# Kernel optimization log

Hardware: AMD Instinct MI355X
Metric: run time of the kernel (lower is better)

The kernel has to match this reference:

```python
import jax, jax.numpy as jnp
import numpy as np
import math

B, P, N, DM, H, DK, DH, DF = 2, 12, 170, 64, 8, 8, 32, 256
SQ = math.sqrt(DK)

def _ln(x, g, b):
    m = jnp.mean(x, -1, keepdims=True)
    v = jnp.var(x, -1, keepdims=True)
    return (x - m) / jnp.sqrt(v + 1e-5) * g + b

def _nozero_softmax(s):
    # faithful to nozero_softmax: mask = (s != 0), max over full row, +1e-5 in denom
    mask = (s != 0).astype(s.dtype)
    e = jnp.exp(s - jnp.max(s, -1, keepdims=True)) * mask
    return e / (jnp.sum(e, -1, keepdims=True) + 1e-5)

def _meta(c, w1, b1, w2, b2):
    # MetaLearner: [B,P,N,DM] -> [3,B,P,N,H,DK,DM]
    h = jax.nn.relu(c @ w1 + b1) @ w2 + b2
    h = h.reshape(c.shape[:3] + (3, H, DK, DM))
    return jnp.moveaxis(h, 3, 0)

def _mhlin(W, x):
    # multihead_linear_transform: per-position meta weight applied to x
    return jnp.einsum('bpnhkd,bpnd->bpnhk', W, x)

def _gdc(data, W1, W2):
    # Gated_Dynamic_Connection (noGC=False). data: [G,B,P,N,C]
    d = jnp.moveaxis(data, 0, 3)  # [B,P,N,G,C]
    a = jnp.einsum('bpngc,gcd->bpngd', d, W1)
    s = jax.nn.softmax(jax.nn.relu(jnp.einsum('bpngc,gcd->bpngd', d, W2)), axis=3)
    return jnp.sum(a * s, axis=3)  # [B,P,N,DM]

def _swish_gate(x, out, wg, bg, wo, bo):
    h = (x @ wg + bg) * out
    return (h * jax.nn.sigmoid(h)) @ wo + bo

def _spatial(Q, K, V, T):
    # adjacency-masked spatial attention. Dense-masked form is exactly the
    # scatter-into-zeros buffer of the original: zero where T==0, QK/sqrt(dk) on edges.
    s = jnp.einsum('bpihk,bpjhk->bphij', Q, K) / SQ
    Tb = T if T.ndim == 2 else T[:, :, None]  # adaptive graph [B,P,1,N,N]
    s = s * (Tb != 0)
    alpha = _nozero_softmax(s) * Tb
    return jnp.einsum('bphij,bpjhk->hbpik', alpha, V)  # [H,B,P,N,DK]

def _temporal(Q, K, V):
    s = jnp.einsum('bqnhk,bpnhk->bnhqp', Q, K) / SQ
    alpha = jax.nn.softmax(s, -1)
    return jnp.einsum('bnhqp,bpnhk->hbqnk', alpha, V)  # [H,B,P,N,DK]

def _retnet(Q, K, V, D):
    # multihead_temporal_regnet with g=1 leading dim folded in
    r = jnp.einsum('bqnhk,bpnhk->bnhqp', Q, K) / SQ
    r = r * D  # D: [H,P,P] causal decay
    rs = jnp.maximum(jnp.abs(jnp.sum(r, -1, keepdims=True)), 1.0)
    r = r / rs
    return jnp.einsum('bnhqp,bpnhk->hbqnk', r, V)  # [H,B,P,N,DK]

def _forward(x, c_x, enc, T, A, D, mr_w1, mr_b1, mr_w2, mr_b2, ms0_w1, ms0_b1, ms0_w2, ms0_b2, ms1_w1, ms1_b1, ms1_w2, ms1_b2, gr_W1, gr_W2, gs0_W1, gs0_W2, gs1_W1, gs1_W2, g2_W1, g2_W2, ge_W1, ge_W2, swr_wg, swr_bg, swr_wo, swr_bo, sws_wg, sws_bg, sws_wo, sws_bo, swe_wg, swe_bg, swe_wo, swe_bo, lnr_g, lnr_b, lns_g, lns_b, lne_g, lne_b, lnf_g, lnf_b, wq, wk, wv, f_w1, f_b1, f_w2, f_b2):
    # 1) RetNet-style temporal self retention (meta-learned QKV)
    W = _meta(c_x, mr_w1, mr_b1, mr_w2, mr_b2)
    o = _gdc(_retnet(_mhlin(W[0], x), _mhlin(W[1], x), _mhlin(W[2], x), D), gr_W1, gr_W2)
    o = _swish_gate(x, o, swr_wg, swr_bg, swr_wo, swr_bo)
    x1 = _ln(o + x, lnr_g, lnr_b)
    # 2) Spatial self attention: predefined graph + adaptive graph branches
    W0 = _meta(c_x, ms0_w1, ms0_b1, ms0_w2, ms0_b2)
    o0 = _gdc(_spatial(_mhlin(W0[0], x1), _mhlin(W0[1], x1), _mhlin(W0[2], x1), T), gs0_W1, gs0_W2)
    W1m = _meta(c_x, ms1_w1, ms1_b1, ms1_w2, ms1_b2)
    o1 = _gdc(_spatial(_mhlin(W1m[0], x1), _mhlin(W1m[1], x1), _mhlin(W1m[2], x1), A), gs1_W1, gs1_W2)
    o = _gdc(jnp.stack([o0, o1], 0), g2_W1, g2_W2)
    o = _swish_gate(x1, o, sws_wg, sws_bg, sws_wo, sws_bo)
    x2 = _ln(o + x1, lns_g, lns_b)
    # 3) Temporal encoder-decoder attention
    q = (x2 @ wq).reshape(B, P, N, H, DK)
    k = (enc @ wk).reshape(B, P, N, H, DK)
    v = (enc @ wv).reshape(B, P, N, H, DK)
    o = _gdc(_temporal(q, k, v), ge_W1, ge_W2)
    o = _swish_gate(x2, o, swe_wg, swe_bg, swe_wo, swe_bo)
    x3 = _ln(o + x2, lne_g, lne_b)
    # 4) FFN
    o = jax.nn.relu(x3 @ f_w1 + f_b1) @ f_w2 + f_b2
    return _ln(o + x3, lnf_g, lnf_b)


def setup_inputs() -> dict:
    key = jax.random.key(0)
    ks = iter(jax.random.split(key, 100))
    def rn(shape, s=0.05):
        return (jax.random.normal(next(ks), shape) * s).astype(jnp.float32)
    inp = {}
    inp['x'] = jax.random.normal(next(ks), (B, P, N, DM), jnp.float32)
    inp['c_x'] = jax.random.normal(next(ks), (B, P, N, DM), jnp.float32)
    inp['enc'] = jax.random.normal(next(ks), (B, P, N, DM), jnp.float32)
    mT = jax.random.uniform(next(ks), (N, N)) < 0.1
    inp['T'] = (jax.random.uniform(next(ks), (N, N)) * mT).astype(jnp.float32)
    mA = jax.random.uniform(next(ks), (B, P, N, N)) < 0.05
    inp['A'] = (jax.random.uniform(next(ks), (B, P, N, N)) * mA).astype(jnp.float32)
    q = np.arange(P)
    gam = 1.0 - 2.0 ** (-5.0 - np.arange(H))
    Dm = np.where(q[:, None] >= q[None, :], gam[:, None, None] ** (q[:, None] - q[None, :]), 0.0)
    inp['D'] = jnp.asarray(Dm, jnp.float32)  # [H,P,P]
    for p in ['mr', 'ms0', 'ms1']:
        inp[p + '_w1'] = rn((DM, DH)); inp[p + '_b1'] = jnp.zeros((DH,), jnp.float32)
        inp[p + '_w2'] = rn((DH, 3 * H * DK * DM)); inp[p + '_b2'] = jnp.zeros((3 * H * DK * DM,), jnp.float32)
    for p in ['gr', 'gs0', 'gs1', 'ge']:
        inp[p + '_W1'] = rn((H, DK, DM)); inp[p + '_W2'] = rn((H, DK, DM))
    inp['g2_W1'] = rn((2, DM, DM)); inp['g2_W2'] = rn((2, DM, DM))
    for p in ['swr', 'sws', 'swe']:
        inp[p + '_wg'] = rn((DM, DM)); inp[p + '_bg'] = jnp.zeros((DM,), jnp.float32)
        inp[p + '_wo'] = rn((DM, DM)); inp[p + '_bo'] = jnp.zeros((DM,), jnp.float32)
    for p in ['lnr', 'lns', 'lne', 'lnf']:
        inp[p + '_g'] = jnp.ones((DM,), jnp.float32); inp[p + '_b'] = jnp.zeros((DM,), jnp.float32)
    inp['wq'] = rn((DM, DM)); inp['wk'] = rn((DM, DM)); inp['wv'] = rn((DM, DM))
    inp['f_w1'] = rn((DM, DF)); inp['f_b1'] = jnp.zeros((DF,), jnp.float32)
    inp['f_w2'] = rn((DF, DM)); inp['f_b2'] = jnp.zeros((DM,), jnp.float32)
    return inp


def reference(x, c_x, enc, T, A, D, mr_w1, mr_b1, mr_w2, mr_b2, ms0_w1, ms0_b1, ms0_w2, ms0_b2, ms1_w1, ms1_b1, ms1_w2, ms1_b2, gr_W1, gr_W2, gs0_W1, gs0_W2, gs1_W1, gs1_W2, g2_W1, g2_W2, ge_W1, ge_W2, swr_wg, swr_bg, swr_wo, swr_bo, sws_wg, sws_bg, sws_wo, sws_bo, swe_wg, swe_bg, swe_wo, swe_bo, lnr_g, lnr_b, lns_g, lns_b, lne_g, lne_b, lnf_g, lnf_b, wq, wk, wv, f_w1, f_b1, f_w2, f_b2):
    return _forward(x, c_x, enc, T, A, D, mr_w1, mr_b1, mr_w2, mr_b2, ms0_w1, ms0_b1, ms0_w2, ms0_b2, ms1_w1, ms1_b1, ms1_w2, ms1_b2, gr_W1, gr_W2, gs0_W1, gs0_W2, gs1_W1, gs1_W2, g2_W1, g2_W2, ge_W1, ge_W2, swr_wg, swr_bg, swr_wo, swr_bo, sws_wg, sws_bg, sws_wo, sws_bo, swe_wg, swe_bg, swe_wo, swe_bo, lnr_g, lnr_b, lns_g, lns_b, lne_g, lne_b, lnf_g, lnf_b, wq, wk, wv, f_w1, f_b1, f_w2, f_b2)
```

## Files before the change

kernel.cpp:

```cpp
#include <hip/hip_runtime.h>
#include <hip/hip_bf16.h>
#include <math.h>

namespace {

constexpr int B_ = 2, P_ = 12, N_ = 170, DM_ = 64, H_ = 8, DK_ = 8, DH_ = 32, DF_ = 256;
constexpr int T_ = B_ * P_ * N_;
constexpr float SQRT_DK = 2.8284271247461903f;

constexpr int NG_ = 12;
constexpr int NC_ = 66;
constexpr int WFRAG_G = NG_ * NC_ * 64 * 8;

typedef __attribute__((ext_vector_type(4))) short short4v;
typedef __attribute__((ext_vector_type(8))) short short8v;
typedef __attribute__((ext_vector_type(4))) float float4v;

__device__ __forceinline__ unsigned short f2bf(float x) {
    union { float f; unsigned int u; } c; c.f = x;
    unsigned int r = (c.u + 0x7FFFu + ((c.u >> 16) & 1u)) >> 16;
    return (unsigned short)r;
}

__global__ void k_pre(const float* __restrict__ c_x,
                      const float* __restrict__ w1a, const float* __restrict__ b1a,
                      const float* __restrict__ w1b, const float* __restrict__ b1b,
                      const float* __restrict__ w1c, const float* __restrict__ b1c,
                      const float* __restrict__ w2a, const float* __restrict__ b2a,
                      const float* __restrict__ w2b, const float* __restrict__ b2b,
                      const float* __restrict__ w2c, const float* __restrict__ b2c,
                      float* __restrict__ hra, float* __restrict__ hrb,
                      float* __restrict__ hrc, unsigned short* __restrict__ Wfrag) {
    if (blockIdx.y == 0) {
        int idx = blockIdx.x * 256 + threadIdx.x;
        if (idx >= 3 * NG_ * NC_ * 64) return;
        int lane = idx & 63;
        int c = (idx >> 6) % NC_;
        int ng = (idx >> 6) / NC_ % NG_;
        int g = idx / (64 * NC_ * NG_);
        const float* w2 = g == 0 ? w2a : (g == 1 ? w2b : w2c);
        const float* b2 = g == 0 ? b2a : (g == 1 ? b2b : b2c);
        int m = ng * 16 + (lane & 15);
        int u = c >> 1;
        int d0 = (c & 1) * 32 + (lane >> 4) * 8;
        const float* src = (u < DH_) ? (w2 + u * 12288 + m * 64 + d0) : (b2 + m * 64 + d0);
        short8v o;
        #pragma unroll
        for (int j = 0; j < 8; ++j) o[j] = (short)f2bf(src[j]);
        *(short8v*)(Wfrag + (size_t)idx * 8) = o;
    } else {
        int z = blockIdx.y - 1;
        const float* w1 = z == 0 ? w1a : (z == 1 ? w1b : w1c);
        const float* b1 = z == 0 ? b1a : (z == 1 ? b1b : b1c);
        float* hr = z == 0 ? hra : (z == 1 ? hrb : hrc);
        int idx = blockIdx.x * 256 + threadIdx.x;
        if (idx >= T_ * DH_) return;
        int t = idx / DH_, j = idx % DH_;
        float acc = b1[j];
        const float* cx = c_x + t * DM_;
        #pragma unroll
        for (int d = 0; d < DM_; ++d) acc += cx[d] * w1[d * DH_ + j];
        hr[idx] = fmaxf(acc, 0.f);
    }
}

__global__ __launch_bounds__(256) void k_meta_gemm2(
    const float* __restrict__ hr0, const float* __restrict__ hr1,
    const float* __restrict__ xin,
    const unsigned short* __restrict__ Wf0, const unsigned short* __restrict__ Wf1,
    float* __restrict__ out0, float* __restrict__ out1) {
    const int bz = blockIdx.z;
    const float* hr = bz ? hr1 : hr0;
    const unsigned short* Wf = bz ? Wf1 : Wf0;
    float* out = bz ? out1 : out0;

    const int tid = threadIdx.x;
    const int wv = tid >> 6, lane = tid & 63;
    const int l15 = lane & 15, quad = lane >> 4;
    const int g16 = blockIdx.x * 4 + wv;
    if (g16 >= 255) return;
    const int t = g16 * 16 + l15;
    const int nb = blockIdx.y;

    const float* xp = xin + t * 64 + quad * 8;
    float4v xa = *(const float4v*)(xp);
    float4v xb = *(const float4v*)(xp + 4);
    float4v xc = *(const float4v*)(xp + 32);
    float4v xd = *(const float4v*)(xp + 36);
    float xr[16] = {xa.x, xa.y, xa.z, xa.w, xb.x, xb.y, xb.z, xb.w,
                    xc.x, xc.y, xc.z, xc.w, xd.x, xd.y, xd.z, xd.w};

    const float* hrp = hr + t * 32;
    float hrbuf[32];
    #pragma unroll
    for (int i = 0; i < 8; ++i) {
        float4v h4 = *(const float4v*)(hrp + i * 4);
        hrbuf[i * 4 + 0] = h4.x; hrbuf[i * 4 + 1] = h4.y;
        hrbuf[i * 4 + 2] = h4.z; hrbuf[i * 4 + 3] = h4.w;
    }

    float4v acc[2] = {{0.f,0.f,0.f,0.f},{0.f,0.f,0.f,0.f}};

    const unsigned short* wb = Wf + ((size_t)(nb * 2) * NC_ * 64 + lane) * 8;
    const size_t qstride = (size_t)NC_ * 64 * 8;
    const size_t cstride = 64 * 8;

    short8v b[2][4];
    {
        const unsigned short* wc = wb;
        #pragma unroll
        for (int q = 0; q < 2; ++q) {
            b[0][2 * q]     = *(const short8v*)(wc + q * qstride);
            b[0][2 * q + 1] = *(const short8v*)(wc + q * qstride + cstride);
        }
    }
    #pragma unroll
    for (int u = 0; u < 33; ++u) {
        const int cur = u & 1, nxt = cur ^ 1;
        if (u + 1 < 33) {
            const unsigned short* wc = wb + (size_t)(2 * (u + 1)) * cstride;
            #pragma unroll
            for (int q = 0; q < 2; ++q) {
                b[nxt][2 * q]     = *(const short8v*)(wc + q * qstride);
                b[nxt][2 * q + 1] = *(const short8v*)(wc + q * qstride + cstride);
            }
        }
        float hrv = (u < 32) ? hrbuf[u] : 1.0f;
        short8v a0, a1;
        #pragma unroll
        for (int j = 0; j < 8; ++j) {
            a0[j] = (short)f2bf(hrv * xr[j]);
            a1[j] = (short)f2bf(hrv * xr[8 + j]);
        }
        #pragma unroll
        for (int q = 0; q < 2; ++q) {
            acc[q] = __builtin_amdgcn_mfma_f32_16x16x32_bf16(a0, b[cur][2 * q],     acc[q], 0, 0, 0);
            acc[q] = __builtin_amdgcn_mfma_f32_16x16x32_bf16(a1, b[cur][2 * q + 1], acc[q], 0, 0, 0);
        }
    }

    #pragma unroll
    for (int q = 0; q < 2; ++q) {
        #pragma unroll
        for (int r = 0; r < 4; ++r) {
            int tt = g16 * 16 + quad * 4 + r;
            out[tt * 192 + nb * 32 + q * 16 + l15] = acc[q][r];
        }
    }
}

__global__ __launch_bounds__(256) void k_retnet(const float* __restrict__ qkv,
                                                const float* __restrict__ Dm,
                                                float* __restrict__ att) {
    const int bn = blockIdx.x;
    const int b = bn / N_, n = bn % N_;
    __shared__ float S[12][192];
    __shared__ float Ds[8 * 145];
    const int tid = threadIdx.x;
    for (int e = tid; e < 12 * 192; e += 256) {
        int p = e / 192, c = e % 192;
        S[p][c] = qkv[((size_t)((b * P_ + p) * N_ + n)) * 192 + c];
    }
    for (int e = tid; e < 1152; e += 256) {
        Ds[(e / 144) * 145 + (e % 144)] = Dm[e];
    }
    __syncthreads();
    const int wv = tid >> 6;
    const int lane = tid & 63;
    const int h = lane >> 3, k = lane & 7;
    const int q = blockIdx.y * 4 + wv;
    float Qv = S[q][h * 8 + k];
    float r[P_];
    float rsum = 0.f;
    #pragma unroll
    for (int p = 0; p < P_; ++p) {
        float prod = Qv * S[p][64 + h * 8 + k];
        prod += __shfl_xor(prod, 1, 64);
        prod += __shfl_xor(prod, 2, 64);
        prod += __shfl_xor(prod, 4, 64);
        float s = (prod / SQRT_DK) * Ds[h * 145 + q * 12 + p];
        r[p] = s; rsum += s;
    }
    float rs = fmaxf(fabsf(rsum), 1.0f);
    float acc = 0.f;
    #pragma unroll
    for (int p = 0; p < P_; ++p) acc += (r[p] / rs) * S[p][128 + h * 8 + k];
    att[((size_t)((b * P_ + q) * N_ + n)) * 64 + lane] = acc;
}

__global__ __launch_bounds__(256) void k_temporal(const float* __restrict__ qkv,
                                                  float* __restrict__ att) {
    const int bn = blockIdx.x;
    const int b = bn / N_, n = bn % N_;
    __shared__ float S[12][192];
    const int tid = threadIdx.x;
    for (int e = tid; e < 12 * 192; e += 256) {
        int p = e / 192, c = e % 192;
        S[p][c] = qkv[((size_t)((b * P_ + p) * N_ + n)) * 192 + c];
    }
    __syncthreads();
    const int wv = tid >> 6;
    const int lane = tid & 63;
    const int h = lane >> 3, k = lane & 7;
    const int q = blockIdx.y * 4 + wv;
    float Qv = S[q][h * 8 + k];
    float s[P_];
    float mx = -1e30f;
    #pragma unroll
    for (int p = 0; p < P_; ++p) {
        float prod = Qv * S[p][64 + h * 8 + k];
        prod += __shfl_xor(prod, 1, 64);
        prod += __shfl_xor(prod, 2, 64);
        prod += __shfl_xor(prod, 4, 64);
        float v = prod / SQRT_DK;
        s[p] = v; mx = fmaxf(mx, v);
    }
    float den = 0.f, acc = 0.f;
    #pragma unroll
    for (int p = 0; p < P_; ++p) {
        float e = expf(s[p] - mx);
        den += e;
        acc += e * S[p][128 + h * 8 + k];
    }
    att[((size_t)((b * P_ + q) * N_ + n)) * 64 + lane] = acc / den;
}

__global__ __launch_bounds__(256) void k_spatial_sparse(
    const float* __restrict__ qkvA, const float* __restrict__ qkvB,
    const float* __restrict__ Tm, const float* __restrict__ Am,
    float* __restrict__ attA, float* __restrict__ attB) {
    const int bp = blockIdx.y;
    const int g = blockIdx.z;
    const float* qkv = g ? qkvB : qkvA;
    float* att = g ? attB : attA;

    __shared__ int2 elist[4][176];

    const int tid = threadIdx.x;
    const int wv = tid >> 6, lane = tid & 63;
    const int i = blockIdx.x * 4 + wv;
    if (i >= N_) return;

    int2* el = elist[wv];
    const float* Trow = g ? (Am + (size_t)(bp * N_ + i) * N_) : (Tm + (size_t)i * N_);
    int nnz = 0;
    #pragma unroll
    for (int c = 0; c < 3; ++c) {
        int j = c * 64 + lane;
        float w = (j < N_) ? Trow[j] : 0.f;
        unsigned long long m = __ballot(w != 0.f);
        if (w != 0.f) {
            int pos = nnz + (int)__popcll(m & ((1ull << lane) - 1ull));
            el[pos] = make_int2(j, __float_as_int(w));
        }
        nnz += (int)__popcll(m);
    }

    const float q = qkv[(size_t)(bp * N_ + i) * 192 + lane];
    float m = 0.f;
    float den = 0.f, acc = 0.f;
    int e = 0;
    for (; e + 1 < nnz; e += 2) {
        int2 e0 = el[e], e1 = el[e + 1];
        const float* r0 = qkv + (size_t)(bp * N_ + e0.x) * 192;
        const float* r1 = qkv + (size_t)(bp * N_ + e1.x) * 192;
        float k0 = r0[64 + lane], v0 = r0[128 + lane];
        float k1 = r1[64 + lane], v1 = r1[128 + lane];
        float p0 = q * k0, p1 = q * k1;
        p0 += __shfl_xor(p0, 1, 64); p1 += __shfl_xor(p1, 1, 64);
        p0 += __shfl_xor(p0, 2, 64); p1 += __shfl_xor(p1, 2, 64);
        p0 += __shfl_xor(p0, 4, 64); p1 += __shfl_xor(p1, 4, 64);
        float s0 = p0 / SQRT_DK, s1 = p1 / SQRT_DK;
        float mn = fmaxf(m, fmaxf(s0, s1));
        float cs = expf(m - mn);
        float x0 = (s0 != 0.f) ? expf(s0 - mn) : 0.f;
        float x1 = (s1 != 0.f) ? expf(s1 - mn) : 0.f;
        den = den * cs + x0 + x1;
        acc = acc * cs + x0 * __int_as_float(e0.y) * v0
                       + x1 * __int_as_float(e1.y) * v1;
        m = mn;
    }
    if (e < nnz) {
        int2 e0 = el[e];
        const float* r0 = qkv + (size_t)(bp * N_ + e0.x) * 192;
        float k0 = r0[64 + lane], v0 = r0[128 + lane];
        float p0 = q * k0;
        p0 += __shfl_xor(p0, 1, 64);
        p0 += __shfl_xor(p0, 2, 64);
        p0 += __shfl_xor(p0, 4, 64);
        float s0 = p0 / SQRT_DK;
        float mn = fmaxf(m, s0);
        float cs = expf(m - mn);
        float x0 = (s0 != 0.f) ? expf(s0 - mn) : 0.f;
        den = den * cs + x0;
        acc = acc * cs + x0 * __int_as_float(e0.y) * v0;
    }

    att[(size_t)(bp * N_ + i) * 64 + lane] = acc / (den + 1e-5f);
}

__device__ __forceinline__ void gdc8x2(const float* dv0, const float* dv1,
                                       const float* W1, const float* W2, int dm,
                                       float& out0, float& out1) {
    float a0[8], s0[8], a1[8], s1[8];
    #pragma unroll
    for (int g = 0; g < 8; ++g) {
        float aa0 = 0.f, ss0 = 0.f, aa1 = 0.f, ss1 = 0.f;
        #pragma unroll
        for (int c = 0; c < 8; ++c) {
            float w1v = W1[(g * 8 + c) * 64 + dm];
            float w2v = W2[(g * 8 + c) * 64 + dm];
            float d0 = dv0[g * 8 + c], d1 = dv1[g * 8 + c];
            aa0 += d0 * w1v; ss0 += d0 * w2v;
            aa1 += d1 * w1v; ss1 += d1 * w2v;
        }
        a0[g] = aa0; s0[g] = fmaxf(ss0, 0.f);
        a1[g] = aa1; s1[g] = fmaxf(ss1, 0.f);
    }
    float mx0 = s0[0], mx1 = s1[0];
    #pragma unroll
    for (int g = 1; g < 8; ++g) { mx0 = fmaxf(mx0, s0[g]); mx1 = fmaxf(mx1, s1[g]); }
    float den0 = 0.f, o0 = 0.f, den1 = 0.f, o1 = 0.f;
    #pragma unroll
    for (int g = 0; g < 8; ++g) {
        float e0 = expf(s0[g] - mx0); den0 += e0; o0 += a0[g] * e0;
        float e1 = expf(s1[g] - mx1); den1 += e1; o1 += a1[g] * e1;
    }
    out0 = o0 / den0; out1 = o1 / den1;
}

__device__ __forceinline__ float ln_out(float r, int dm, const float* g, const float* b) {
    float m = r, m2 = r * r;
    #pragma unroll
    for (int off = 32; off; off >>= 1) { m += __shfl_xor(m, off, 64); m2 += __shfl_xor(m2, off, 64); }
    m *= (1.f / 64.f); m2 *= (1.f / 64.f);
    float var = m2 - m * m;
    return (r - m) * rsqrtf(var + 1e-5f) * g[dm] + b[dm];
}

__global__ __launch_bounds__(64) void k_gsl(const float* __restrict__ att,
    const float* __restrict__ xin,
    const float* W1, const float* W2,
    const float* wg, const float* bg,
    const float* wo, const float* bo,
    const float* lng, const float* lnb, float* __restrict__ xout) {
    const int t0 = blockIdx.x * 2, dm = threadIdx.x;
    __shared__ float dv0[64], dv1[64], xv0[64], xv1[64], sw0[64], sw1[64];
    dv0[dm] = att[t0 * 64 + dm];       dv1[dm] = att[t0 * 64 + 64 + dm];
    xv0[dm] = xin[t0 * 64 + dm];       xv1[dm] = xin[t0 * 64 + 64 + dm];
    __syncthreads();
    float o0, o1;
    gdc8x2(dv0, dv1, W1, W2, dm, o0, o1);
    float hg0 = bg[dm], hg1 = hg0;
    #pragma unroll
    for (int d = 0; d < 64; ++d) {
        float w = wg[d * 64 + dm];
        hg0 += xv0[d] * w; hg1 += xv1[d] * w;
    }
    hg0 *= o0; hg1 *= o1;
    sw0[dm] = hg0 / (1.f + expf(-hg0));
    sw1[dm] = hg1 / (1.f + expf(-hg1));
    __syncthreads();
    float ov0 = bo[dm], ov1 = ov0;
    #pragma unroll
    for (int d = 0; d < 64; ++d) {
        float w = wo[d * 64 + dm];
        ov0 += sw0[d] * w; ov1 += sw1[d] * w;
    }
    xout[t0 * 64 + dm]      = ln_out(ov0 + xv0[dm], dm, lng, lnb);
    xout[t0 * 64 + 64 + dm] = ln_out(ov1 + xv1[dm], dm, lng, lnb);
}

__global__ __launch_bounds__(64) void k_spatial_fuse_qkv(
    const float* __restrict__ att0, const float* __restrict__ att1,
    const float* __restrict__ x1,
    const float* gs0_W1, const float* gs0_W2,
    const float* gs1_W1, const float* gs1_W2,
    const float* g2_W1, const float* g2_W2,
    const float* wg, const float* bg,
    const float* wo, const float* bo,
    const float* lng, const float* lnb,
    const float* __restrict__ enc,
    const float* wqm, const float* wkm, const float* wvm,
    float* __restrict__ x2f, float* __restrict__ qkv) {
    const int t0 = blockIdx.x * 2, dm = threadIdx.x;
    __shared__ float d00[64], d01[64], d10[64], d11[64];
    __shared__ float xv0[64], xv1[64], ev0[64], ev1[64];
    __shared__ float o00[64], o01[64], o10[64], o11[64];
    __shared__ float sw0[64], sw1[64], x20[64], x21[64];
    d00[dm] = att0[t0 * 64 + dm];  d01[dm] = att0[t0 * 64 + 64 + dm];
    d10[dm] = att1[t0 * 64 + dm];  d11[dm] = att1[t0 * 64 + 64 + dm];
    xv0[dm] = x1[t0 * 64 + dm];    xv1[dm] = x1[t0 * 64 + 64 + dm];
    ev0[dm] = enc[t0 * 64 + dm];   ev1[dm] = enc[t0 * 64 + 64 + dm];
    __syncthreads();
    float g00, g01, g10, g11;
    gdc8x2(d00, d01, gs0_W1, gs0_W2, dm, g00, g01);
    gdc8x2(d10, d11, gs1_W1, gs1_W2, dm, g10, g11);
    o00[dm] = g00; o01[dm] = g01; o10[dm] = g10; o11[dm] = g11;
    __syncthreads();
    float a0t0 = 0.f, s0t0 = 0.f, a1t0 = 0.f, s1t0 = 0.f;
    float a0t1 = 0.f, s0t1 = 0.f, a1t1 = 0.f, s1t1 = 0.f;
    #pragma unroll
    for (int c = 0; c < 64; ++c) {
        float wA0 = g2_W1[c * 64 + dm],        wS0 = g2_W2[c * 64 + dm];
        float wA1 = g2_W1[(64 + c) * 64 + dm], wS1 = g2_W2[(64 + c) * 64 + dm];
        float v00 = o00[c], v01 = o01[c], v10 = o10[c], v11 = o11[c];
        a0t0 += v00 * wA0; s0t0 += v00 * wS0; a1t0 += v10 * wA1; s1t0 += v10 * wS1;
        a0t1 += v01 * wA0; s0t1 += v01 * wS0; a1t1 += v11 * wA1; s1t1 += v11 * wS1;
    }
    float o_t0, o_t1;
    {
        float p = fmaxf(s0t0, 0.f), qv = fmaxf(s1t0, 0.f);
        float mx = fmaxf(p, qv);
        float e0 = expf(p - mx), e1 = expf(qv - mx);
        o_t0 = (a0t0 * e0 + a1t0 * e1) / (e0 + e1);
    }
    {
        float p = fmaxf(s0t1, 0.f), qv = fmaxf(s1t1, 0.f);
        float mx = fmaxf(p, qv);
        float e0 = expf(p - mx), e1 = expf(qv - mx);
        o_t1 = (a0t1 * e0 + a1t1 * e1) / (e0 + e1);
    }
    float hg0 = bg[dm], hg1 = hg0;
    #pragma unroll
    for (int d = 0; d < 64; ++d) {
        float w = wg[d * 64 + dm];
        hg0 += xv0[d] * w; hg1 += xv1[d] * w;
    }
    hg0 *= o_t0; hg1 *= o_t1;
    sw0[dm] = hg0 / (1.f + expf(-hg0));
    sw1[dm] = hg1 / (1.f + expf(-hg1));
    __syncthreads();
    float ov0 = bo[dm], ov1 = ov0;
    #pragma unroll
    for (int d = 0; d < 64; ++d) {
        float w = wo[d * 64 + dm];
        ov0 += sw0[d] * w; ov1 += sw1[d] * w;
    }
    float r0 = ln_out(ov0 + xv0[dm], dm, lng, lnb);
    float r1 = ln_out(ov1 + xv1[dm], dm, lng, lnb);
    x2f[t0 * 64 + dm] = r0;       x2f[t0 * 64 + 64 + dm] = r1;
    x20[dm] = r0;                 x21[dm] = r1;
    __syncthreads();
    float aq0 = 0.f, ak0 = 0.f, av0 = 0.f, aq1 = 0.f, ak1 = 0.f, av1 = 0.f;
    #pragma unroll
    for (int d = 0; d < 64; ++d) {
        float wq_ = wqm[d * 64 + dm];
        float wk_ = wkm[d * 64 + dm];
        float wv_ = wvm[d * 64 + dm];
        aq0 += x20[d] * wq_; aq1 += x21[d] * wq_;
        ak0 += ev0[d] * wk_; ak1 += ev1[d] * wk_;
        av0 += ev0[d] * wv_; av1 += ev1[d] * wv_;
    }
    qkv[t0 * 192 + dm] = aq0;
    qkv[t0 * 192 + 64 + dm] = ak0;
    qkv[t0 * 192 + 128 + dm] = av0;
    qkv[(t0 + 1) * 192 + dm] = aq1;
    qkv[(t0 + 1) * 192 + 64 + dm] = ak1;
    qkv[(t0 + 1) * 192 + 128 + dm] = av1;
}

__global__ __launch_bounds__(64) void k_gsl_ffn(const float* __restrict__ att,
    const float* __restrict__ xin,
    const float* W1, const float* W2,
    const float* wg, const float* bg,
    const float* wo, const float* bo,
    const float* lng, const float* lnb,
    const float* w1, const float* b1,
    const float* w2, const float* b2,
    const float* lnfg, const float* lnfb,
    float* __restrict__ out) {
    const int t0 = blockIdx.x * 2, dm = threadIdx.x;
    __shared__ float dv0[64], dv1[64], xv0[64], xv1[64], sw0[64], sw1[64];
    __shared__ float x30[64], x31[64], hv0[256], hv1[256];
    dv0[dm] = att[t0 * 64 + dm];   dv1[dm] = att[t0 * 64 + 64 + dm];
    xv0[dm] = xin[t0 * 64 + dm];   xv1[dm] = xin[t0 * 64 + 64 + dm];
    __syncthreads();
    float o0, o1;
    gdc8x2(dv0, dv1, W1, W2, dm, o0, o1);
    float hg0 = bg[dm], hg1 = hg0;
    #pragma unroll
    for (int d = 0; d < 64; ++d) {
        float w = wg[d * 64 + dm];
        hg0 += xv0[d] * w; hg1 += xv1[d] * w;
    }
    hg0 *= o0; hg1 *= o1;
    sw0[dm] = hg0 / (1.f + expf(-hg0));
    sw1[dm] = hg1 / (1.f + expf(-hg1));
    __syncthreads();
    float ov0 = bo[dm], ov1 = ov0;
    #pragma unroll
    for (int d = 0; d < 64; ++d) {
        float w = wo[d * 64 + dm];
        ov0 += sw0[d] * w; ov1 += sw1[d] * w;
    }
    float x3_0 = ln_out(ov0 + xv0[dm], dm, lng, lnb);
    float x3_1 = ln_out(ov1 + xv1[dm], dm, lng, lnb);
    x30[dm] = x3_0; x31[dm] = x3_1;
    __syncthreads();
    #pragma unroll
    for (int e = 0; e < 4; ++e) {
        int j = e * 64 + dm;
        float a0 = b1[j], a1 = a0;
        #pragma unroll
        for (int d = 0; d < 64; ++d) {
            float w = w1[d * 256 + j];
            a0 += x30[d] * w; a1 += x31[d] * w;
        }
        hv0[j] = fmaxf(a0, 0.f);
        hv1[j] = fmaxf(a1, 0.f);
    }
    __syncthreads();
    float a0 = b2[dm], a1 = a0;
    for (int j = 0; j < 256; ++j) {
        float w = w2[j * 64 + dm];
        a0 += hv0[j] * w; a1 += hv1[j] * w;
    }
    out[t0 * 64 + dm]      = ln_out(a0 + x3_0, dm, lnfg, lnfb);
    out[t0 * 64 + 64 + dm] = ln_out(a1 + x3_1, dm, lnfg, lnfb);
}

}

extern "C" void kernel_launch(void* const* d_in, const int* in_sizes, int n_in,
                              void* d_out, int out_size, void* d_ws, size_t ws_size,
                              hipStream_t stream) {
    (void)in_sizes; (void)n_in; (void)out_size; (void)ws_size;
    const float* x    = (const float*)d_in[0];
    const float* c_x  = (const float*)d_in[1];
    const float* enc  = (const float*)d_in[2];
    const float* Tm   = (const float*)d_in[3];
    const float* Am   = (const float*)d_in[4];
    const float* Dm   = (const float*)d_in[5];
    const float* mr_w1 = (const float*)d_in[6];
    const float* mr_b1 = (const float*)d_in[7];
    const float* mr_w2 = (const float*)d_in[8];
    const float* mr_b2 = (const float*)d_in[9];
    const float* ms0_w1 = (const float*)d_in[10];
    const float* ms0_b1 = (const float*)d_in[11];
    const float* ms0_w2 = (const float*)d_in[12];
    const float* ms0_b2 = (const float*)d_in[13];
    const float* ms1_w1 = (const float*)d_in[14];
    const float* ms1_b1 = (const float*)d_in[15];
    const float* ms1_w2 = (const float*)d_in[16];
    const float* ms1_b2 = (const float*)d_in[17];
    const float* gr_W1 = (const float*)d_in[18];
    const float* gr_W2 = (const float*)d_in[19];
    const float* gs0_W1 = (const float*)d_in[20];
    const float* gs0_W2 = (const float*)d_in[21];
    const float* gs1_W1 = (const float*)d_in[22];
    const float* gs1_W2 = (const float*)d_in[23];
    const float* g2_W1 = (const float*)d_in[24];
    const float* g2_W2 = (const float*)d_in[25];
    const float* ge_W1 = (const float*)d_in[26];
    const float* ge_W2 = (const float*)d_in[27];
    const float* swr_wg = (const float*)d_in[28];
    const float* swr_bg = (const float*)d_in[29];
    const float* swr_wo = (const float*)d_in[30];
    const float* swr_bo = (const float*)d_in[31];
    const float* sws_wg = (const float*)d_in[32];
    const float* sws_bg = (const float*)d_in[33];
    const float* sws_wo = (const float*)d_in[34];
    const float* sws_bo = (const float*)d_in[35];
    const float* swe_wg = (const float*)d_in[36];
    const float* swe_bg = (const float*)d_in[37];
    const float* swe_wo = (const float*)d_in[38];
    const float* swe_bo = (const float*)d_in[39];
    const float* lnr_g = (const float*)d_in[40];
    const float* lnr_b = (const float*)d_in[41];
    const float* lns_g = (const float*)d_in[42];
    const float* lns_b = (const float*)d_in[43];
    const float* lne_g = (const float*)d_in[44];
    const float* lne_b = (const float*)d_in[45];
    const float* lnf_g = (const float*)d_in[46];
    const float* lnf_b = (const float*)d_in[47];
    const float* wq = (const float*)d_in[48];
    const float* wk = (const float*)d_in[49];
    const float* wv = (const float*)d_in[50];
    const float* f_w1 = (const float*)d_in[51];
    const float* f_b1 = (const float*)d_in[52];
    const float* f_w2 = (const float*)d_in[53];
    const float* f_b2 = (const float*)d_in[54];

    float* ws   = (float*)d_ws;
    float* hr   = ws;
    float* hr2  = hr   + T_ * DH_;
    float* qkva = hr2  + T_ * DH_;
    float* qkvb = qkva + T_ * 192;
    float* atta = qkvb + T_ * 192;
    float* attb = atta + T_ * DM_;
    float* x1f  = attb + T_ * DM_;
    float* x2f  = x1f  + T_ * DM_;
    float* x3f  = x2f  + T_ * DM_;
    unsigned short* Wfrag = (unsigned short*)(x3f + T_ * DM_);
    float* hr_r = attb;

    k_pre<<<dim3(594, 4), 256, 0, stream>>>(
        c_x, mr_w1, mr_b1, ms0_w1, ms0_b1, ms1_w1, ms1_b1,
        mr_w2, mr_b2, ms0_w2, ms0_b2, ms1_w2, ms1_b2,
        hr_r, hr, hr2, Wfrag);

    k_meta_gemm2<<<dim3(64, 6, 1), 256, 0, stream>>>(
        hr_r, hr_r, x, Wfrag, Wfrag, qkva, qkva);
    k_retnet<<<dim3(B_ * N_, 3), 256, 0, stream>>>(qkva, Dm, atta);
    k_gsl<<<T_ / 2, 64, 0, stream>>>(atta, x, gr_W1, gr_W2, swr_wg, swr_bg,
                                     swr_wo, swr_bo, lnr_g, lnr_b, x1f);

    k_meta_gemm2<<<dim3(64, 6, 2), 256, 0, stream>>>(
        hr, hr2, x1f, Wfrag + WFRAG_G, Wfrag + 2 * WFRAG_G, qkva, qkvb);
    k_spatial_sparse<<<dim3((N_ + 3) / 4, B_ * P_, 2), 256, 0, stream>>>(
        qkva, qkvb, Tm, Am, atta, attb);
    k_spatial_fuse_qkv<<<T_ / 2, 64, 0, stream>>>(atta, attb, x1f,
        gs0_W1, gs0_W2, gs1_W1, gs1_W2, g2_W1, g2_W2,
        sws_wg, sws_bg, sws_wo, sws_bo, lns_g, lns_b,
        enc, wq, wk, wv, x2f, qkva);

    k_temporal<<<dim3(B_ * N_, 3), 256, 0, stream>>>(qkva, atta);
    k_gsl_ffn<<<T_ / 2, 64, 0, stream>>>(atta, x2f, ge_W1, ge_W2, swe_wg, swe_bg,
                                         swe_wo, swe_bo, lne_g, lne_b,
                                         f_w1, f_b1, f_w2, f_b2, lnf_g, lnf_b,
                                         (float*)d_out);
}
```

Baseline: 299.6 us.

## Process four tokens per block in GSL kernels and merge temporal query blocks

The per-token fused kernels (k_gsl, k_spatial_fuse_qkv, k_gsl_ffn) now handle four tokens per 64-thread block instead of two. Each weight element loaded from global memory is reused across twice as many tokens, which halves weight traffic per token. The retnet and temporal kernels now run one 768-thread block per (b,n) covering all 12 queries, instead of three 256-thread blocks that each reloaded the same 12x192 tile. The cost is more registers and LDS per block and half as many blocks, which could lower occupancy and latency hiding.

```diff
diff --git a/kernel.cpp b/kernel.cpp
--- a/kernel.cpp
+++ b/kernel.cpp
@@ -149,7 +149,7 @@
     }
 }
 
-__global__ __launch_bounds__(256) void k_retnet(const float* __restrict__ qkv,
+__global__ __launch_bounds__(768) void k_retnet(const float* __restrict__ qkv,
                                                 const float* __restrict__ Dm,
                                                 float* __restrict__ att) {
     const int bn = blockIdx.x;
@@ -157,18 +157,17 @@
     __shared__ float S[12][192];
     __shared__ float Ds[8 * 145];
     const int tid = threadIdx.x;
-    for (int e = tid; e < 12 * 192; e += 256) {
+    for (int e = tid; e < 12 * 192; e += 768) {
         int p = e / 192, c = e % 192;
         S[p][c] = qkv[((size_t)((b * P_ + p) * N_ + n)) * 192 + c];
     }
-    for (int e = tid; e < 1152; e += 256) {
+    for (int e = tid; e < 1152; e += 768) {
         Ds[(e / 144) * 145 + (e % 144)] = Dm[e];
     }
     __syncthreads();
-    const int wv = tid >> 6;
+    const int q = tid >> 6;
     const int lane = tid & 63;
     const int h = lane >> 3, k = lane & 7;
-    const int q = blockIdx.y * 4 + wv;
     float Qv = S[q][h * 8 + k];
     float r[P_];
     float rsum = 0.f;
@@ -188,21 +187,20 @@
     att[((size_t)((b * P_ + q) * N_ + n)) * 64 + lane] = acc;
 }
 
-__global__ __launch_bounds__(256) void k_temporal(const float* __restrict__ qkv,
+__global__ __launch_bounds__(768) void k_temporal(const float* __restrict__ qkv,
                                                   float* __restrict__ att) {
     const int bn = blockIdx.x;
     const int b = bn / N_, n = bn % N_;
     __shared__ float S[12][192];
     const int tid = threadIdx.x;
-    for (int e = tid; e < 12 * 192; e += 256) {
+    for (int e = tid; e < 12 * 192; e += 768) {
         int p = e / 192, c = e % 192;
         S[p][c] = qkv[((size_t)((b * P_ + p) * N_ + n)) * 192 + c];
     }
     __syncthreads();
-    const int wv = tid >> 6;
+    const int q = tid >> 6;
     const int lane = tid & 63;
     const int h = lane >> 3, k = lane & 7;
-    const int q = blockIdx.y * 4 + wv;
     float Qv = S[q][h * 8 + k];
     float s[P_];
     float mx = -1e30f;
@@ -299,34 +297,47 @@
     att[(size_t)(bp * N_ + i) * 64 + lane] = acc / (den + 1e-5f);
 }
 
-__device__ __forceinline__ void gdc8x2(const float* dv0, const float* dv1,
+__device__ __forceinline__ void gdc8x4(const float* dv0, const float* dv1,
+                                       const float* dv2, const float* dv3,
                                        const float* W1, const float* W2, int dm,
-                                       float& out0, float& out1) {
-    float a0[8], s0[8], a1[8], s1[8];
+                                       float& r0, float& r1, float& r2, float& r3) {
+    float a0[8], s0[8], a1[8], s1[8], a2[8], s2[8], a3[8], s3[8];
     #pragma unroll
     for (int g = 0; g < 8; ++g) {
         float aa0 = 0.f, ss0 = 0.f, aa1 = 0.f, ss1 = 0.f;
+        float aa2 = 0.f, ss2 = 0.f, aa3 = 0.f, ss3 = 0.f;
         #pragma unroll
         for (int c = 0; c < 8; ++c) {
             float w1v = W1[(g * 8 + c) * 64 + dm];
             float w2v = W2[(g * 8 + c) * 64 + dm];
             float d0 = dv0[g * 8 + c], d1 = dv1[g * 8 + c];
+            float d2 = dv2[g * 8 + c], d3 = dv3[g * 8 + c];
             aa0 += d0 * w1v; ss0 += d0 * w2v;
             aa1 += d1 * w1v; ss1 += d1 * w2v;
+            aa2 += d2 * w1v; ss2 += d2 * w2v;
+            aa3 += d3 * w1v; ss3 += d3 * w2v;
         }
         a0[g] = aa0; s0[g] = fmaxf(ss0, 0.f);
         a1[g] = aa1; s1[g] = fmaxf(ss1, 0.f);
-    }
-    float mx0 = s0[0], mx1 = s1[0];
-    #pragma unroll
-    for (int g = 1; g < 8; ++g) { mx0 = fmaxf(mx0, s0[g]); mx1 = fmaxf(mx1, s1[g]); }
+        a2[g] = aa2; s2[g] = fmaxf(ss2, 0.f);
+        a3[g] = aa3; s3[g] = fmaxf(ss3, 0.f);
+    }
+    float mx0 = s0[0], mx1 = s1[0], mx2 = s2[0], mx3 = s3[0];
+    #pragma unroll
+    for (int g = 1; g < 8; ++g) {
+        mx0 = fmaxf(mx0, s0[g]); mx1 = fmaxf(mx1, s1[g]);
+        mx2 = fmaxf(mx2, s2[g]); mx3 = fmaxf(mx3, s3[g]);
+    }
     float den0 = 0.f, o0 = 0.f, den1 = 0.f, o1 = 0.f;
+    float den2 = 0.f, o2 = 0.f, den3 = 0.f, o3 = 0.f;
     #pragma unroll
     for (int g = 0; g < 8; ++g) {
         float e0 = expf(s0[g] - mx0); den0 += e0; o0 += a0[g] * e0;
         float e1 = expf(s1[g] - mx1); den1 += e1; o1 += a1[g] * e1;
-    }
-    out0 = o0 / den0; out1 = o1 / den1;
+        float e2 = expf(s2[g] - mx2); den2 += e2; o2 += a2[g] * e2;
+        float e3 = expf(s3[g] - mx3); den3 += e3; o3 += a3[g] * e3;
+    }
+    r0 = o0 / den0; r1 = o1 / den1; r2 = o2 / den2; r3 = o3 / den3;
 }
 
 __device__ __forceinline__ float ln_out(float r, int dm, const float* g, const float* b) {
@@ -344,31 +355,40 @@
     const float* wg, const float* bg,
     const float* wo, const float* bo,
     const float* lng, const float* lnb, float* __restrict__ xout) {
-    const int t0 = blockIdx.x * 2, dm = threadIdx.x;
-    __shared__ float dv0[64], dv1[64], xv0[64], xv1[64], sw0[64], sw1[64];
-    dv0[dm] = att[t0 * 64 + dm];       dv1[dm] = att[t0 * 64 + 64 + dm];
-    xv0[dm] = xin[t0 * 64 + dm];       xv1[dm] = xin[t0 * 64 + 64 + dm];
-    __syncthreads();
-    float o0, o1;
-    gdc8x2(dv0, dv1, W1, W2, dm, o0, o1);
-    float hg0 = bg[dm], hg1 = hg0;
+    const int t0 = blockIdx.x * 4, dm = threadIdx.x;
+    __shared__ float dv[4][64], xv[4][64], sw[4][64];
+    #pragma unroll
+    for (int s = 0; s < 4; ++s) {
+        dv[s][dm] = att[(t0 + s) * 64 + dm];
+        xv[s][dm] = xin[(t0 + s) * 64 + dm];
+    }
+    __syncthreads();
+    float o0, o1, o2, o3;
+    gdc8x4(dv[0], dv[1], dv[2], dv[3], W1, W2, dm, o0, o1, o2, o3);
+    float hg0 = bg[dm], hg1 = hg0, hg2 = hg0, hg3 = hg0;
     #pragma unroll
     for (int d = 0; d < 64; ++d) {
         float w = wg[d * 64 + dm];
-        hg0 += xv0[d] * w; hg1 += xv1[d] * w;
-    }
-    hg0 *= o0; hg1 *= o1;
-    sw0[dm] = hg0 / (1.f + expf(-hg0));
-    sw1[dm] = hg1 / (1.f + expf(-hg1));
-    __syncthreads();
-    float ov0 = bo[dm], ov1 = ov0;
+        hg0 += xv[0][d] * w; hg1 += xv[1][d] * w;
+        hg2 += xv[2][d] * w; hg3 += xv[3][d] * w;
+    }
+    hg0 *= o0; hg1 *= o1; hg2 *= o2; hg3 *= o3;
+    sw[0][dm] = hg0 / (1.f + expf(-hg0));
+    sw[1][dm] = hg1 / (1.f + expf(-hg1));
+    sw[2][dm] = hg2 / (1.f + expf(-hg2));
+    sw[3][dm] = hg3 / (1.f + expf(-hg3));
+    __syncthreads();
+    float ov0 = bo[dm], ov1 = ov0, ov2 = ov0, ov3 = ov0;
     #pragma unroll
     for (int d = 0; d < 64; ++d) {
         float w = wo[d * 64 + dm];
-        ov0 += sw0[d] * w; ov1 += sw1[d] * w;
-    }
-    xout[t0 * 64 + dm]      = ln_out(ov0 + xv0[dm], dm, lng, lnb);
-    xout[t0 * 64 + 64 + dm] = ln_out(ov1 + xv1[dm], dm, lng, lnb);
+        ov0 += sw[0][d] * w; ov1 += sw[1][d] * w;
+        ov2 += sw[2][d] * w; ov3 += sw[3][d] * w;
+    }
+    xout[(t0 + 0) * 64 + dm] = ln_out(ov0 + xv[0][dm], dm, lng, lnb);
+    xout[(t0 + 1) * 64 + dm] = ln_out(ov1 + xv[1][dm], dm, lng, lnb);
+    xout[(t0 + 2) * 64 + dm] = ln_out(ov2 + xv[2][dm], dm, lng, lnb);
+    xout[(t0 + 3) * 64 + dm] = ln_out(ov3 + xv[3][dm], dm, lng, lnb);
 }
 
 __global__ __launch_bounds__(64) void k_spatial_fuse_qkv(
@@ -383,81 +403,91 @@
     const float* __restrict__ enc,
     const float* wqm, const float* wkm, const float* wvm,
     float* __restrict__ x2f, float* __restrict__ qkv) {
-    const int t0 = blockIdx.x * 2, dm = threadIdx.x;
-    __shared__ float d00[64], d01[64], d10[64], d11[64];
-    __shared__ float xv0[64], xv1[64], ev0[64], ev1[64];
-    __shared__ float o00[64], o01[64], o10[64], o11[64];
-    __shared__ float sw0[64], sw1[64], x20[64], x21[64];
-    d00[dm] = att0[t0 * 64 + dm];  d01[dm] = att0[t0 * 64 + 64 + dm];
-    d10[dm] = att1[t0 * 64 + dm];  d11[dm] = att1[t0 * 64 + 64 + dm];
-    xv0[dm] = x1[t0 * 64 + dm];    xv1[dm] = x1[t0 * 64 + 64 + dm];
-    ev0[dm] = enc[t0 * 64 + dm];   ev1[dm] = enc[t0 * 64 + 64 + dm];
-    __syncthreads();
-    float g00, g01, g10, g11;
-    gdc8x2(d00, d01, gs0_W1, gs0_W2, dm, g00, g01);
-    gdc8x2(d10, d11, gs1_W1, gs1_W2, dm, g10, g11);
-    o00[dm] = g00; o01[dm] = g01; o10[dm] = g10; o11[dm] = g11;
-    __syncthreads();
-    float a0t0 = 0.f, s0t0 = 0.f, a1t0 = 0.f, s1t0 = 0.f;
-    float a0t1 = 0.f, s0t1 = 0.f, a1t1 = 0.f, s1t1 = 0.f;
+    const int t0 = blockIdx.x * 4, dm = threadIdx.x;
+    __shared__ float d0s[4][64], d1s[4][64], xv[4][64], ev[4][64];
+    __shared__ float o0s[4][64], o1s[4][64], sw[4][64], x2s[4][64];
+    #pragma unroll
+    for (int s = 0; s < 4; ++s) {
+        d0s[s][dm] = att0[(t0 + s) * 64 + dm];
+        d1s[s][dm] = att1[(t0 + s) * 64 + dm];
+        xv[s][dm]  = x1[(t0 + s) * 64 + dm];
+        ev[s][dm]  = enc[(t0 + s) * 64 + dm];
+    }
+    __syncthreads();
+    float g0[4], g1[4];
+    gdc8x4(d0s[0], d0s[1], d0s[2], d0s[3], gs0_W1, gs0_W2, dm, g0[0], g0[1], g0[2], g0[3]);
+    gdc8x4(d1s[0], d1s[1], d1s[2], d1s[3], gs1_W1, gs1_W2, dm, g1[0], g1[1], g1[2], g1[3]);
+    #pragma unroll
+    for (int s = 0; s < 4; ++s) { o0s[s][dm] = g0[s]; o1s[s][dm] = g1[s]; }
+    __syncthreads();
+    float aA[4] = {0.f, 0.f, 0.f, 0.f}, sA[4] = {0.f, 0.f, 0.f, 0.f};
+    float aB[4] = {0.f, 0.f, 0.f, 0.f}, sB[4] = {0.f, 0.f, 0.f, 0.f};
     #pragma unroll
     for (int c = 0; c < 64; ++c) {
         float wA0 = g2_W1[c * 64 + dm],        wS0 = g2_W2[c * 64 + dm];
         float wA1 = g2_W1[(64 + c) * 64 + dm], wS1 = g2_W2[(64 + c) * 64 + dm];
-        float v00 = o00[c], v01 = o01[c], v10 = o10[c], v11 = o11[c];
-        a0t0 += v00 * wA0; s0t0 += v00 * wS0; a1t0 += v10 * wA1; s1t0 += v10 * wS1;
-        a0t1 += v01 * wA0; s0t1 += v01 * wS0; a1t1 += v11 * wA1; s1t1 += v11 * wS1;
-    }
-    float o_t0, o_t1;
-    {
-        float p = fmaxf(s0t0, 0.f), qv = fmaxf(s1t0, 0.f);
+        #pragma unroll
+        for (int s = 0; s < 4; ++s) {
+            float v0 = o0s[s][c], v1 = o1s[s][c];
+            aA[s] += v0 * wA0; sA[s] += v0 * wS0;
+            aB[s] += v1 * wA1; sB[s] += v1 * wS1;
+        }
+    }
+    float og[4];
+    #pragma unroll
+    for (int s = 0; s < 4; ++s) {
+        float p = fmaxf(sA[s], 0.f), qv = fmaxf(sB[s], 0.f);
         float mx = fmaxf(p, qv);
         float e0 = expf(p - mx), e1 = expf(qv - mx);
-        o_t0 = (a0t0 * e0 + a1t0 * e1) / (e0 + e1);
-    }
-    {
-        float p = fmaxf(s0t1, 0.f), qv = fmaxf(s1t1, 0.f);
-        float mx = fmaxf(p, qv);
-        float e0 = expf(p - mx), e1 = expf(qv - mx);
-        o_t1 = (a0t1 * e0 + a1t1 * e1) / (e0 + e1);
-    }
-    float hg0 = bg[dm], hg1 = hg0;
+        og[s] = (aA[s] * e0 + aB[s] * e1) / (e0 + e1);
+    }
+    float hg[4] = {bg[dm], bg[dm], bg[dm], bg[dm]};
     #pragma unroll
     for (int d = 0; d < 64; ++d) {
         float w = wg[d * 64 + dm];
-        hg0 += xv0[d] * w; hg1 += xv1[d] * w;
-    }
-    hg0 *= o_t0; hg1 *= o_t1;
-    sw0[dm] = hg0 / (1.f + expf(-hg0));
-    sw1[dm] = hg1 / (1.f + expf(-hg1));
-    __syncthreads();
-    float ov0 = bo[dm], ov1 = ov0;
+        #pragma unroll
+        for (int s = 0; s < 4; ++s) hg[s] += xv[s][d] * w;
+    }
+    #pragma unroll
+    for (int s = 0; s < 4; ++s) {
+        float h = hg[s] * og[s];
+        sw[s][dm] = h / (1.f + expf(-h));
+    }
+    __syncthreads();
+    float ov[4] = {bo[dm], bo[dm], bo[dm], bo[dm]};
     #pragma unroll
     for (int d = 0; d < 64; ++d) {
         float w = wo[d * 64 + dm];
-        ov0 += sw0[d] * w; ov1 += sw1[d] * w;
-    }
-    float r0 = ln_out(ov0 + xv0[dm], dm, lng, lnb);
-    float r1 = ln_out(ov1 + xv1[dm], dm, lng, lnb);
-    x2f[t0 * 64 + dm] = r0;       x2f[t0 * 64 + 64 + dm] = r1;
-    x20[dm] = r0;                 x21[dm] = r1;
-    __syncthreads();
-    float aq0 = 0.f, ak0 = 0.f, av0 = 0.f, aq1 = 0.f, ak1 = 0.f, av1 = 0.f;
+        #pragma unroll
+        for (int s = 0; s < 4; ++s) ov[s] += sw[s][d] * w;
+    }
+    float x2r[4];
+    #pragma unroll
+    for (int s = 0; s < 4; ++s) {
+        x2r[s] = ln_out(ov[s] + xv[s][dm], dm, lng, lnb);
+        x2f[(t0 + s) * 64 + dm] = x2r[s];
+        x2s[s][dm] = x2r[s];
+    }
+    __syncthreads();
+    float aq[4] = {0.f, 0.f, 0.f, 0.f}, ak[4] = {0.f, 0.f, 0.f, 0.f}, av[4] = {0.f, 0.f, 0.f, 0.f};
     #pragma unroll
     for (int d = 0; d < 64; ++d) {
         float wq_ = wqm[d * 64 + dm];
         float wk_ = wkm[d * 64 + dm];
         float wv_ = wvm[d * 64 + dm];
-        aq0 += x20[d] * wq_; aq1 += x21[d] * wq_;
-        ak0 += ev0[d] * wk_; ak1 += ev1[d] * wk_;
-        av0 += ev0[d] * wv_; av1 += ev1[d] * wv_;
-    }
-    qkv[t0 * 192 + dm] = aq0;
-    qkv[t0 * 192 + 64 + dm] = ak0;
-    qkv[t0 * 192 + 128 + dm] = av0;
-    qkv[(t0 + 1) * 192 + dm] = aq1;
-    qkv[(t0 + 1) * 192 + 64 + dm] = ak1;
-    qkv[(t0 + 1) * 192 + 128 + dm] = av1;
+        #pragma unroll
+        for (int s = 0; s < 4; ++s) {
+            aq[s] += x2s[s][d] * wq_;
+            ak[s] += ev[s][d] * wk_;
+            av[s] += ev[s][d] * wv_;
+        }
+    }
+    #pragma unroll
+    for (int s = 0; s < 4; ++s) {
+        qkv[(t0 + s) * 192 + dm] = aq[s];
+        qkv[(t0 + s) * 192 + 64 + dm] = ak[s];
+        qkv[(t0 + s) * 192 + 128 + dm] = av[s];
+    }
 }
 
 __global__ __launch_bounds__(64) void k_gsl_ffn(const float* __restrict__ att,
@@ -470,54 +500,71 @@
     const float* w2, const float* b2,
     const float* lnfg, const float* lnfb,
     float* __restrict__ out) {
-    const int t0 = blockIdx.x * 2, dm = threadIdx.x;
-    __shared__ float dv0[64], dv1[64], xv0[64], xv1[64], sw0[64], sw1[64];
-    __shared__ float x30[64], x31[64], hv0[256], hv1[256];
-    dv0[dm] = att[t0 * 64 + dm];   dv1[dm] = att[t0 * 64 + 64 + dm];
-    xv0[dm] = xin[t0 * 64 + dm];   xv1[dm] = xin[t0 * 64 + 64 + dm];
-    __syncthreads();
-    float o0, o1;
-    gdc8x2(dv0, dv1, W1, W2, dm, o0, o1);
-    float hg0 = bg[dm], hg1 = hg0;
+    const int t0 = blockIdx.x * 4, dm = threadIdx.x;
+    __shared__ float dv[4][64], xv[4][64], sw[4][64];
+    __shared__ float x3s[4][64], hv[4][256];
+    #pragma unroll
+    for (int s = 0; s < 4; ++s) {
+        dv[s][dm] = att[(t0 + s) * 64 + dm];
+        xv[s][dm] = xin[(t0 + s) * 64 + dm];
+    }
+    __syncthreads();
+    float o0, o1, o2, o3;
+    gdc8x4(dv[0], dv[1], dv[2], dv[3], W1, W2, dm, o0, o1, o2, o3);
+    float hg0 = bg[dm], hg1 = hg0, hg2 = hg0, hg3 = hg0;
     #pragma unroll
     for (int d = 0; d < 64; ++d) {
         float w = wg[d * 64 + dm];
-        hg0 += xv0[d] * w; hg1 += xv1[d] * w;
-    }
-    hg0 *= o0; hg1 *= o1;
-    sw0[dm] = hg0 / (1.f + expf(-hg0));
-    sw1[dm] = hg1 / (1.f + expf(-hg1));
-    __syncthreads();
-    float ov0 = bo[dm], ov1 = ov0;
+        hg0 += xv[0][d] * w; hg1 += xv[1][d] * w;
+        hg2 += xv[2][d] * w; hg3 += xv[3][d] * w;
+    }
+    hg0 *= o0; hg1 *= o1; hg2 *= o2; hg3 *= o3;
+    sw[0][dm] = hg0 / (1.f + expf(-hg0));
+    sw[1][dm] = hg1 / (1.f + expf(-hg1));
+    sw[2][dm] = hg2 / (1.f + expf(-hg2));
+    sw[3][dm] = hg3 / (1.f + expf(-hg3));
+    __syncthreads();
+    float ov0 = bo[dm], ov1 = ov0, ov2 = ov0, ov3 = ov0;
     #pragma unroll
     for (int d = 0; d < 64; ++d) {
         float w = wo[d * 64 + dm];
-        ov0 += sw0[d] * w; ov1 += sw1[d] * w;
-    }
-    float x3_0 = ln_out(ov0 + xv0[dm], dm, lng, lnb);
-    float x3_1 = ln_out(ov1 + xv1[dm], dm, lng, lnb);
-    x30[dm] = x3_0; x31[dm] = x3_1;
+        ov0 += sw[0][d] * w; ov1 += sw[1][d] * w;
+        ov2 += sw[2][d] * w; ov3 += sw[3][d] * w;
+    }
+    float x3r[4];
+    x3r[0] = ln_out(ov0 + xv[0][dm], dm, lng, lnb);
+    x3r[1] = ln_out(ov1 + xv[1][dm], dm, lng, lnb);
+    x3r[2] = ln_out(ov2 + xv[2][dm], dm, lng, lnb);
+    x3r[3] = ln_out(ov3 + xv[3][dm], dm, lng, lnb);
+    #pragma unroll
+    for (int s = 0; s < 4; ++s) x3s[s][dm] = x3r[s];
     __syncthreads();
     #pragma unroll
     for (int e = 0; e < 4; ++e) {
         int j = e * 64 + dm;
-        float a0 = b1[j], a1 = a0;
+        float a0 = b1[j], a1 = a0, a2 = a0, a3 = a0;
         #pragma unroll
         for (int d = 0; d < 64; ++d) {
             float w = w1[d * 256 + j];
-            a0 += x30[d] * w; a1 += x31[d] * w;
-        }
-        hv0[j] = fmaxf(a0, 0.f);
-        hv1[j] = fmaxf(a1, 0.f);
-    }
-    __syncthreads();
-    float a0 = b2[dm], a1 = a0;
+            a0 += x3s[0][d] * w; a1 += x3s[1][d] * w;
+            a2 += x3s[2][d] * w; a3 += x3s[3][d] * w;
+        }
+        hv[0][j] = fmaxf(a0, 0.f);
+        hv[1][j] = fmaxf(a1, 0.f);
+        hv[2][j] = fmaxf(a2, 0.f);
+        hv[3][j] = fmaxf(a3, 0.f);
+    }
+    __syncthreads();
+    float a0 = b2[dm], a1 = a0, a2 = a0, a3 = a0;
     for (int j = 0; j < 256; ++j) {
         float w = w2[j * 64 + dm];
-        a0 += hv0[j] * w; a1 += hv1[j] * w;
-    }
-    out[t0 * 64 + dm]      = ln_out(a0 + x3_0, dm, lnfg, lnfb);
-    out[t0 * 64 + 64 + dm] = ln_out(a1 + x3_1, dm, lnfg, lnfb);
+        a0 += hv[0][j] * w; a1 += hv[1][j] * w;
+        a2 += hv[2][j] * w; a3 += hv[3][j] * w;
+    }
+    out[(t0 + 0) * 64 + dm] = ln_out(a0 + x3r[0], dm, lnfg, lnfb);
+    out[(t0 + 1) * 64 + dm] = ln_out(a1 + x3r[1], dm, lnfg, lnfb);
+    out[(t0 + 2) * 64 + dm] = ln_out(a2 + x3r[2], dm, lnfg, lnfb);
+    out[(t0 + 3) * 64 + dm] = ln_out(a3 + x3r[3], dm, lnfg, lnfb);
 }
 
 }
@@ -602,21 +649,21 @@
 
     k_meta_gemm2<<<dim3(64, 6, 1), 256, 0, stream>>>(
         hr_r, hr_r, x, Wfrag, Wfrag, qkva, qkva);
-    k_retnet<<<dim3(B_ * N_, 3), 256, 0, stream>>>(qkva, Dm, atta);
-    k_gsl<<<T_ / 2, 64, 0, stream>>>(atta, x, gr_W1, gr_W2, swr_wg, swr_bg,
+    k_retnet<<<B_ * N_, 768, 0, stream>>>(qkva, Dm, atta);
+    k_gsl<<<T_ / 4, 64, 0, stream>>>(atta, x, gr_W1, gr_W2, swr_wg, swr_bg,
                                      swr_wo, swr_bo, lnr_g, lnr_b, x1f);
 
     k_meta_gemm2<<<dim3(64, 6, 2), 256, 0, stream>>>(
         hr, hr2, x1f, Wfrag + WFRAG_G, Wfrag + 2 * WFRAG_G, qkva, qkvb);
     k_spatial_sparse<<<dim3((N_ + 3) / 4, B_ * P_, 2), 256, 0, stream>>>(
         qkva, qkvb, Tm, Am, atta, attb);
-    k_spatial_fuse_qkv<<<T_ / 2, 64, 0, stream>>>(atta, attb, x1f,
+    k_spatial_fuse_qkv<<<T_ / 4, 64, 0, stream>>>(atta, attb, x1f,
         gs0_W1, gs0_W2, gs1_W1, gs1_W2, g2_W1, g2_W2,
         sws_wg, sws_bg, sws_wo, sws_bo, lns_g, lns_b,
         enc, wq, wk, wv, x2f, qkva);
 
-    k_temporal<<<dim3(B_ * N_, 3), 256, 0, stream>>>(qkva, atta);
-    k_gsl_ffn<<<T_ / 2, 64, 0, stream>>>(atta, x2f, ge_W1, ge_W2, swe_wg, swe_bg,
+    k_temporal<<<B_ * N_, 768, 0, stream>>>(qkva, atta);
+    k_gsl_ffn<<<T_ / 4, 64, 0, stream>>>(atta, x2f, ge_W1, ge_W2, swe_wg, swe_bg,
                                          swe_wo, swe_bo, lne_g, lne_b,
                                          f_w1, f_b1, f_w2, f_b2, lnf_g, lnf_b,
                                          (float*)d_out);
```

After: 372.6 us. 24.3% more time.
